# Kernel optimization log

Hardware: AMD Instinct MI355X
Metric: run time of the kernel (lower is better)

## Reference

```python
import jax, jax.numpy as jnp
import numpy as np

B, S, D = 2, 11253, 256
NHEAD, NLEVEL, DFF = 8, 4, 1024
KERNEL = 2
NPOINT = KERNEL * KERNEL
HEAD_DIM = D // NHEAD
LEVEL_SHAPES = [(92, 92), (46, 46), (23, 23), (12, 12)]
LEVEL_STARTS = np.cumsum([0] + [h * w for h, w in LEVEL_SHAPES])[:-1]


def _kernel_indices():
    # BoxeR _create_kernel_indices: even kernel -> [-0.5, 0.5]/K, (x, y) order
    idx = np.arange(KERNEL, dtype=np.float32) - (KERNEL - 1) / 2.0
    i, j = np.meshgrid(idx, idx, indexing="ij")
    return jnp.asarray(np.stack([j, i], -1).reshape(-1, 2) / KERNEL)


KIDX = _kernel_indices()  # (NPOINT, 2) box-relative sample offsets


def layer_norm(x, w, b, eps=1e-5):
    mu = x.mean(-1, keepdims=True)
    var = ((x - mu) ** 2).mean(-1, keepdims=True)
    return (x - mu) * jax.lax.rsqrt(var + eps) * w + b


def setup_inputs() -> dict:
    key = jax.random.key(0)
    ks = jax.random.split(key, 12)

    def p(i, shape, scale=0.02):
        return jax.random.normal(ks[i], shape, jnp.float32) * scale

    cxcy = jax.random.uniform(ks[2], (B, S, 2), jnp.float32, minval=0.1, maxval=0.9)
    wh = jax.random.uniform(ks[3], (B, S, 2), jnp.float32, minval=0.02, maxval=0.2)
    return dict(
        src=jax.random.normal(ks[0], (B, S, D), jnp.float32),
        pos=jax.random.normal(ks[1], (B, S, D), jnp.float32),
        src_shape=jnp.asarray(np.array(LEVEL_SHAPES, np.int32)),
        src_mask=jnp.zeros((B, S), jnp.bool_),
        src_start_index=jnp.asarray(LEVEL_STARTS.astype(np.int32)),
        src_valid_ratios=jnp.ones((B, NLEVEL, 2), jnp.float32),
        ref_windows=jnp.concatenate([cxcy, wh], -1),
        value_w=p(4, (D, D)), value_b=jnp.zeros((D,), jnp.float32),
        out_w=p(5, (D, D)), out_b=jnp.zeros((D,), jnp.float32),
        box_w=p(6, (NHEAD * NLEVEL * 4, D)), box_b=jnp.zeros((NHEAD * NLEVEL * 4,), jnp.float32),
        attn_w=p(7, (NHEAD * NLEVEL * NPOINT, D)), attn_b=jnp.zeros((NHEAD * NLEVEL * NPOINT,), jnp.float32),
        lin1_w=p(8, (DFF, D)), lin1_b=jnp.zeros((DFF,), jnp.float32),
        lin2_w=p(9, (D, DFF)), lin2_b=jnp.zeros((D,), jnp.float32),
        norm1_w=jnp.ones((D,), jnp.float32), norm1_b=jnp.zeros((D,), jnp.float32),
        norm2_w=jnp.ones((D,), jnp.float32), norm2_b=jnp.zeros((D,), jnp.float32),
    )


def box_attention(q, src, src_mask, src_valid_ratios, ref_windows,
                  value_w, value_b, out_w, out_b, box_w, box_b, attn_w, attn_b):
    value = src @ value_w.T + value_b
    value = jnp.where(src_mask[..., None], 0.0, value)
    value = value.reshape(B, S, NHEAD, HEAD_DIM)

    # where-to-attend: per-head, per-level box offsets decoded around ref_windows (cx,cy,w,h)
    off = (q @ box_w.T + box_b).reshape(B, S, NHEAD, NLEVEL, 4)
    ref = ref_windows[:, :, None, None, :]
    boxes = ref + off / 8.0 * ref[..., jnp.array([2, 3, 2, 3])]
    center, size = boxes[..., None, :2], boxes[..., None, 2:]
    grid = center + KIDX * jax.nn.relu(size)  # (B,S,nh,L,P,2) in normalized [0,1] coords
    grid = grid * src_valid_ratios[:, None, None, :, None, :]

    attn = (q @ attn_w.T + attn_b).reshape(B, S, NHEAD, NLEVEL * NPOINT)
    attn = jax.nn.softmax(attn, -1).reshape(B, S, NHEAD, NLEVEL, NPOINT)

    out = jnp.zeros((B, NHEAD, S, HEAD_DIM), src.dtype)
    for lvl, (H, W) in enumerate(LEVEL_SHAPES):
        s0 = int(LEVEL_STARTS[lvl])
        v = jnp.transpose(value[:, s0:s0 + H * W], (0, 2, 1, 3))  # (B,nh,HW,hd)
        loc = jnp.transpose(grid[:, :, :, lvl], (0, 2, 1, 3, 4))  # (B,nh,S,P,2)
        # grid_sample bilinear, align_corners=False, zero padding
        px = loc[..., 0] * W - 0.5
        py = loc[..., 1] * H - 0.5
        x0, y0 = jnp.floor(px), jnp.floor(py)
        wx, wy = (px - x0)[..., None], (py - y0)[..., None]

        def gather(ix, iy):
            valid = (ix >= 0) & (ix < W) & (iy >= 0) & (iy < H)
            idx = (jnp.clip(iy, 0, H - 1) * W + jnp.clip(ix, 0, W - 1)).astype(jnp.int32)
            g = jnp.take_along_axis(v, idx.reshape(B, NHEAD, S * NPOINT)[..., None], axis=2)
            return g.reshape(B, NHEAD, S, NPOINT, HEAD_DIM) * valid[..., None]

        g00, g01 = gather(x0, y0), gather(x0 + 1, y0)
        g10, g11 = gather(x0, y0 + 1), gather(x0 + 1, y0 + 1)
        samp = (g00 * (1 - wx) + g01 * wx) * (1 - wy) + (g10 * (1 - wx) + g11 * wx) * wy
        aw = jnp.transpose(attn[:, :, :, lvl], (0, 2, 1, 3))  # (B,nh,S,P)
        out = out + jnp.einsum("bhspd,bhsp->bhsd", samp, aw)

    out = jnp.transpose(out, (0, 2, 1, 3)).reshape(B, S, D)
    return out @ out_w.T + out_b


def reference(src, pos, src_shape, src_mask, src_start_index, src_valid_ratios,
              ref_windows, value_w, value_b, out_w, out_b, box_w, box_b,
              attn_w, attn_b, lin1_w, lin1_b, lin2_w, lin2_b,
              norm1_w, norm1_b, norm2_w, norm2_b):
    # self-attn (box attention) + residual + LN
    src2 = box_attention(src + pos, src, src_mask, src_valid_ratios, ref_windows,
                         value_w, value_b, out_w, out_b, box_w, box_b, attn_w, attn_b)
    x = layer_norm(src + src2, norm1_w, norm1_b)
    # FFN + residual + LN (dropout=0 in eval)
    ff = jax.nn.relu(x @ lin1_w.T + lin1_b) @ lin2_w.T + lin2_b
    return layer_norm(x + ff, norm2_w, norm2_b)
```

## Files before the change

### kernel.cpp

```cpp
#include <hip/hip_runtime.h>
#include <hip/hip_bf16.h>
#include <hip/hip_fp16.h>

#define TOKENS 22506
#define SLEN   11253

typedef __bf16 bf16x8 __attribute__((ext_vector_type(8)));
typedef float  f32x4  __attribute__((ext_vector_type(4)));
typedef float  f32x2  __attribute__((ext_vector_type(2)));
typedef uint   u32x4  __attribute__((ext_vector_type(4)));
typedef uint   u32x2  __attribute__((ext_vector_type(2)));

#if defined(__has_builtin)
#if __has_builtin(__builtin_amdgcn_cvt_pk_f32_fp8) && __has_builtin(__builtin_amdgcn_cvt_pk_fp8_f32)
#define HAS_FP8CVT 1
#endif
#endif

__device__ __forceinline__ ushort f2bu(float f) {
    __hip_bfloat16 h = __float2bfloat16(f);
    return *reinterpret_cast<ushort*>(&h);
}
__device__ __forceinline__ float bu2f(ushort u) {
    return __uint_as_float((uint)u << 16);
}
__device__ __forceinline__ uint pkf16(float a, float b) {
    __half2 h = __floats2half2_rn(a, b);
    return *reinterpret_cast<uint*>(&h);
}
__device__ __forceinline__ void gl16(const void* g, void* l) {
    __builtin_amdgcn_global_load_lds(
        (__attribute__((address_space(1))) void*)(g),
        (__attribute__((address_space(3))) void*)(l), 16, 0, 0);
}

#ifndef HAS_FP8CVT
__device__ __forceinline__ uint enc_fp8(float x) {
    if (!(fabsf(x) >= 0.f)) return 0;
    uint u = __float_as_uint(x);
    uint s = (u >> 24) & 0x80u;
    float ax = fabsf(x);
    if (ax >= 448.f) return s | 0x7Eu;
    if (ax < 0.0009765625f) return s;
    int e; frexpf(ax, &e);
    int ue = e - 1;
    if (ue < -6) {
        int m = (int)(ax * 512.f + 0.5f);
        if (m > 7) m = 7;
        return s | (uint)m;
    }
    float q = ax * exp2f((float)(3 - ue));
    int mi = (int)(q + 0.5f);
    if (mi >= 16) { mi >>= 1; ++ue; if (ue > 8) return s | 0x7Eu; }
    return s | ((uint)(ue + 7) << 3) | ((uint)mi & 7u);
}
__device__ __forceinline__ float dec_fp8(uint b) {
    const float sgn = (b & 0x80u) ? -1.f : 1.f;
    const uint e = (b >> 3) & 15u, m = b & 7u;
    if (e == 0) return sgn * (float)m * 0.001953125f;
    return sgn * (1.0f + (float)m * 0.125f) * exp2f((float)e - 7.f);
}
#endif

__device__ __forceinline__ uint fp8pack4(float f0, float f1, float f2, float f3) {
#ifdef HAS_FP8CVT
    int p = 0;
    p = __builtin_amdgcn_cvt_pk_fp8_f32(f0, f1, p, false);
    p = __builtin_amdgcn_cvt_pk_fp8_f32(f2, f3, p, true);
    return (uint)p;
#else
    return enc_fp8(f0) | (enc_fp8(f1) << 8) | (enc_fp8(f2) << 16) | (enc_fp8(f3) << 24);
#endif
}
__device__ __forceinline__ uint fp8pack1(float f) {
#ifdef HAS_FP8CVT
    return (uint)__builtin_amdgcn_cvt_pk_fp8_f32(f, f, 0, false) & 0xFFu;
#else
    return enc_fp8(f);
#endif
}
template<bool HI>
__device__ __forceinline__ f32x2 fp8pair(uint w) {
#ifdef HAS_FP8CVT
    auto c = __builtin_amdgcn_cvt_pk_f32_fp8((int)w, HI);
    f32x2 r; r.x = c[0]; r.y = c[1]; return r;
#else
    const uint sh = HI ? 16u : 0u;
    f32x2 r; r.x = dec_fp8((w >> sh) & 0xFFu); r.y = dec_fp8((w >> (sh + 8)) & 0xFFu);
    return r;
#endif
}

__device__ __forceinline__ void xcd_swz(int& bx, int& by) {
    const int nx = gridDim.x, ny = gridDim.y;
    if ((nx & 7) == 0) {
        const int L = blockIdx.x + nx * blockIdx.y;
        const int chunk = nx >> 3;
        const int k = L & 7, j = L >> 3;
        bx = k * chunk + (j % chunk);
        by = j / chunk;
        if (by >= ny) { bx = blockIdx.x; by = blockIdx.y; }
    } else {
        bx = blockIdx.x; by = blockIdx.y;
    }
}

template<bool RELU, bool NTSTORE, bool F8Z0>
__global__ __launch_bounds__(256) void gemm_small(
    const ushort* __restrict__ A0, const ushort* __restrict__ W0,
    const float* __restrict__ b0, void* __restrict__ C0,
    const ushort* __restrict__ A1, const ushort* __restrict__ W1,
    const float* __restrict__ b1, void* __restrict__ C1,
    int M, int N, int K)
{
    const bool zz = blockIdx.z != 0;
    const ushort* A   = zz ? A1 : A0;
    const ushort* W   = zz ? W1 : W0;
    const float* bias = zz ? b1 : b0;
    void* Cptr        = zz ? C1 : C0;

    __shared__ ushort smem[12288];
    const int tid  = threadIdx.x;
    const int lane = tid & 63;
    const int wid  = tid >> 6;
    const int wr = wid >> 1, wc = wid & 1;
    int bx, by; xcd_swz(bx, by);
    const int m0 = bx * 64, n0 = by * 128;
    const int lrow = lane & 15, lhi = lane >> 4;

    const int arow = tid >> 2;
    const int scol = (tid & 3) << 3;
    const ushort* ga  = A + (size_t)min(m0 + arow, M - 1) * K + scol;
    const ushort* gb0 = W + (size_t)(n0 + arow)      * K + scol;
    const ushort* gb1 = W + (size_t)(n0 + arow + 64) * K + scol;

    f32x4 acc[2][4] = {};
    const int NT = K >> 5;

    gl16(ga,  &smem[tid * 8]);
    gl16(gb0, &smem[4096 + tid * 8]);
    gl16(gb1, &smem[4096 + tid * 8 + 2048]);

    int cur = 0;
    for (int t = 0; t < NT; ++t) {
        __syncthreads();
        if (t + 1 < NT) {
            const int k0 = (t + 1) << 5;
            const int nb = cur ^ 1;
            gl16(ga  + k0, &smem[nb * 2048 + tid * 8]);
            gl16(gb0 + k0, &smem[4096 + nb * 4096 + tid * 8]);
            gl16(gb1 + k0, &smem[4096 + nb * 4096 + tid * 8 + 2048]);
        }
        bf16x8 afr[2], bfr[4];
        #pragma unroll
        for (int m = 0; m < 2; ++m)
            afr[m] = *reinterpret_cast<const bf16x8*>(
                &smem[cur * 2048 + (wr * 32 + m * 16 + lrow) * 32 + lhi * 8]);
        #pragma unroll
        for (int n = 0; n < 4; ++n)
            bfr[n] = *reinterpret_cast<const bf16x8*>(
                &smem[4096 + cur * 4096 + (wc * 64 + n * 16 + lrow) * 32 + lhi * 8]);
        #pragma unroll
        for (int m = 0; m < 2; ++m)
            #pragma unroll
            for (int n = 0; n < 4; ++n)
                acc[m][n] = __builtin_amdgcn_mfma_f32_16x16x32_bf16(
                    afr[m], bfr[n], acc[m][n], 0, 0, 0);
        cur ^= 1;
    }

    __syncthreads();
    #pragma unroll
    for (int m = 0; m < 2; ++m) {
        #pragma unroll
        for (int n = 0; n < 4; ++n) {
            const int col = wc * 64 + n * 16 + lrow;
            const float bv = bias[n0 + col];
            #pragma unroll
            for (int r = 0; r < 4; ++r) {
                const int row = wr * 32 + m * 16 + lhi * 4 + r;
                float v = acc[m][n][r] + bv;
                if (RELU) v = fmaxf(v, 0.f);
                smem[row * 136 + col] = f2bu(v);
            }
        }
    }
    __syncthreads();
    if (F8Z0 && !zz) {
        #pragma unroll
        for (int i = 0; i < 4; ++i) {
            const int e = tid + i * 256;
            const int row = e >> 4, ch = e & 15;
            if (m0 + row < M) {
                const u32x4 v = *reinterpret_cast<const u32x4*>(&smem[row * 136 + ch * 8]);
                float f[8];
                #pragma unroll
                for (int j = 0; j < 4; ++j) {
                    f[2 * j]     = __uint_as_float(v[j] << 16);
                    f[2 * j + 1] = __uint_as_float(v[j] & 0xFFFF0000u);
                }
                u32x2 o;
                o[0] = fp8pack4(f[0], f[1], f[2], f[3]);
                o[1] = fp8pack4(f[4], f[5], f[6], f[7]);
                u32x2* dst = reinterpret_cast<u32x2*>(
                    (unsigned char*)Cptr + (size_t)(m0 + row) * N + n0 + ch * 8);
                if (NTSTORE) __builtin_nontemporal_store(o, dst);
                else *dst = o;
            }
        }
    } else {
        #pragma unroll
        for (int i = 0; i < 4; ++i) {
            const int e = tid + i * 256;
            const int row = e >> 4, ch = e & 15;
            if (m0 + row < M) {
                const u32x4 v = *reinterpret_cast<const u32x4*>(&smem[row * 136 + ch * 8]);
                u32x4* dst = reinterpret_cast<u32x4*>(
                    (ushort*)Cptr + (size_t)(m0 + row) * N + n0 + ch * 8);
                if (NTSTORE) __builtin_nontemporal_store(v, dst);
                else *dst = v;
            }
        }
    }
}

__global__ __launch_bounds__(256) void gemm_f8(
    const unsigned char* __restrict__ A, const unsigned char* __restrict__ W,
    const float* __restrict__ bias, ushort* __restrict__ C,
    int M, int N, int K)
{
    __shared__ unsigned char smem[17408];
    const int tid  = threadIdx.x;
    const int lane = tid & 63;
    const int wid  = tid >> 6;
    const int wr = wid >> 1, wc = wid & 1;
    int bx, by; xcd_swz(bx, by);
    const int m0 = bx * 64, n0 = by * 128;
    const int lrow = lane & 15, lhi = lane >> 4;

    const int arow = tid >> 1;
    const int achk = (tid & 1) << 4;
    const unsigned char* ga = A + (size_t)min(m0 + (arow & 63), M - 1) * K + achk;
    const unsigned char* gb = W + (size_t)(n0 + arow) * K + achk;

    f32x4 acc[2][4] = {};
    const int NT = K >> 5;

    if (tid < 128) gl16(ga, &smem[tid * 16]);
    gl16(gb, &smem[4096 + tid * 16]);

    int cur = 0;
    for (int t = 0; t < NT; ++t) {
        __syncthreads();
        if (t + 1 < NT) {
            const int k0 = (t + 1) << 5;
            const int nb = cur ^ 1;
            if (tid < 128) gl16(ga + k0, &smem[nb * 2048 + tid * 16]);
            gl16(gb + k0, &smem[4096 + nb * 4096 + tid * 16]);
        }
        long afr[2], bfr[4];
        #pragma unroll
        for (int m = 0; m < 2; ++m)
            afr[m] = *reinterpret_cast<const long*>(
                &smem[cur * 2048 + (wr * 32 + m * 16 + lrow) * 32 + lhi * 8]);
        #pragma unroll
        for (int n = 0; n < 4; ++n)
            bfr[n] = *reinterpret_cast<const long*>(
                &smem[4096 + cur * 4096 + (wc * 64 + n * 16 + lrow) * 32 + lhi * 8]);
        #pragma unroll
        for (int m = 0; m < 2; ++m)
            #pragma unroll
            for (int n = 0; n < 4; ++n)
                acc[m][n] = __builtin_amdgcn_mfma_f32_16x16x32_fp8_fp8(
                    afr[m], bfr[n], acc[m][n], 0, 0, 0);
        cur ^= 1;
    }

    __syncthreads();
    ushort* sm16 = reinterpret_cast<ushort*>(smem);
    #pragma unroll
    for (int m = 0; m < 2; ++m) {
        #pragma unroll
        for (int n = 0; n < 4; ++n) {
            const int col = wc * 64 + n * 16 + lrow;
            const float bv = bias[n0 + col];
            #pragma unroll
            for (int r = 0; r < 4; ++r) {
                const int row = wr * 32 + m * 16 + lhi * 4 + r;
                sm16[row * 136 + col] = f2bu(acc[m][n][r] + bv);
            }
        }
    }
    __syncthreads();
    #pragma unroll
    for (int i = 0; i < 4; ++i) {
        const int e = tid + i * 256;
        const int row = e >> 4, ch = e & 15;
        if (m0 + row < M) {
            const u32x4 v = *reinterpret_cast<const u32x4*>(&sm16[row * 136 + ch * 8]);
            *reinterpret_cast<u32x4*>(C + (size_t)(m0 + row) * N + n0 + ch * 8) = v;
        }
    }
}

__global__ __launch_bounds__(256) void prep_all(
    const float* __restrict__ vw, const float* __restrict__ bw,
    const float* __restrict__ aw, const float* __restrict__ ow,
    const float* __restrict__ l1, const float* __restrict__ l2,
    const float* __restrict__ bb, const float* __restrict__ ab,
    ushort* __restrict__ dstW, float* __restrict__ dstQB,
    unsigned char* __restrict__ dstW8,
    const float4* __restrict__ src, const float4* __restrict__ pos,
    ushort4* __restrict__ srcb, ushort4* __restrict__ qb)
{
    const int blk = blockIdx.x;
    if (blk < 2817) {
        const int i = blk * 256 + threadIdx.x;
        if (i < 720896) {
            float v;
            if      (i <  65536) v = vw[i];
            else if (i <  98304) v = bw[i -  65536];
            else if (i < 131072) v = aw[i -  98304];
            else if (i < 196608) v = ow[i - 131072];
            else if (i < 458752) v = l1[i - 196608];
            else                 v = l2[i - 458752];
            dstW[i] = f2bu(v);
            if (i >= 458752) dstW8[i - 458752] = (unsigned char)fp8pack1(v);
        } else if (i < 721152) {
            const int j = i - 720896;
            dstQB[j] = (j < 128) ? bb[j] : ab[j - 128];
        }
    } else {
        const int i = (blk - 2817) * 256 + threadIdx.x;
        if (i >= TOKENS * 64) return;
        const float4 s = src[i], p = pos[i];
        ushort4 us, uq;
        us.x = f2bu(s.x); us.y = f2bu(s.y); us.z = f2bu(s.z); us.w = f2bu(s.w);
        uq.x = f2bu(s.x + p.x); uq.y = f2bu(s.y + p.y);
        uq.z = f2bu(s.z + p.z); uq.w = f2bu(s.w + p.w);
        srcb[i] = us; qb[i] = uq;
    }
}

__global__ __launch_bounds__(256) void box_fused(
    const unsigned char* __restrict__ val,
    const ushort* __restrict__ qout,
    const float* __restrict__ refw,
    const float* __restrict__ vratio,
    ushort* __restrict__ attnout)
{
    __shared__ ushort4 offs[64 * 17];
    __shared__ uint2 wts[64 * 17];
    const int tid = threadIdx.x;

    int work;
    {
        const int x = blockIdx.x & 7, s = blockIdx.x >> 3;
        work = (x < 4) ? (s * 4 + x) : (1408 + s * 4 + (x - 4));
        if ((int)gridDim.x != 2814 || work >= (int)gridDim.x) work = blockIdx.x;
    }
    const int t0 = work * 8;

    {
        const int u = tid >> 2, lvl = tid & 3;
        const int t = min(t0 + (u >> 3), TOKENS - 1);
        const int h = u & 7;
        const int b = (t >= SLEN) ? 1 : 0;
        const ushort* qr = qout + (size_t)t * 256;

        const uint2 lu = *reinterpret_cast<const uint2*>(qr + 128 + h * 16 + lvl * 4);
        float e0 = __uint_as_float(lu.x << 16);
        float e1 = __uint_as_float(lu.x & 0xFFFF0000u);
        float e2 = __uint_as_float(lu.y << 16);
        float e3 = __uint_as_float(lu.y & 0xFFFF0000u);
        float mx = fmaxf(fmaxf(e0, e1), fmaxf(e2, e3));
        mx = fmaxf(mx, __shfl_xor(mx, 1));
        mx = fmaxf(mx, __shfl_xor(mx, 2));
        e0 = __expf(e0 - mx); e1 = __expf(e1 - mx);
        e2 = __expf(e2 - mx); e3 = __expf(e3 - mx);
        float ss = e0 + e1 + e2 + e3;
        ss += __shfl_xor(ss, 1);
        ss += __shfl_xor(ss, 2);
        const float inv = 1.f / ss;
        const float pe[4] = { e0 * inv, e1 * inv, e2 * inv, e3 * inv };

        const uint2 ou = *reinterpret_cast<const uint2*>(qr + h * 16 + lvl * 4);
        const float o0 = __uint_as_float(ou.x << 16) * 0.125f;
        const float o1 = __uint_as_float(ou.x & 0xFFFF0000u) * 0.125f;
        const float o2 = __uint_as_float(ou.y << 16) * 0.125f;
        const float o3 = __uint_as_float(ou.y & 0xFFFF0000u) * 0.125f;

        const float4 rw = *reinterpret_cast<const float4*>(refw + (size_t)t * 4);
        const int Ww = (lvl == 0) ? 92 : (lvl == 1) ? 46 : (lvl == 2) ? 23 : 12;
        const int s0 = (lvl == 0) ? 0 : (lvl == 1) ? 8464 : (lvl == 2) ? 10580 : 11109;
        const float vrx = vratio[(b * 4 + lvl) * 2 + 0];
        const float vry = vratio[(b * 4 + lvl) * 2 + 1];

        const float bx  = rw.x + o0 * rw.z;
        const float by  = rw.y + o1 * rw.w;
        const float bwd = fmaxf(rw.z + o2 * rw.z, 0.f);
        const float bhd = fmaxf(rw.w + o3 * rw.w, 0.f);

        #pragma unroll
        for (int k = 0; k < 4; ++k) {
            const float jx = (k & 1) ? 0.25f : -0.25f;
            const float iy = (k & 2) ? 0.25f : -0.25f;
            const float px = (bx + jx * bwd) * vrx * (float)Ww - 0.5f;
            const float py = (by + iy * bhd) * vry * (float)Ww - 0.5f;
            const float x0f = floorf(px), y0f = floorf(py);
            const int x0 = (int)x0f, y0 = (int)y0f;
            const float wx = px - x0f, wy = py - y0f;
            const float wp = pe[k];

            const bool vx0 = (x0 >= 0) && (x0 < Ww);
            const bool vx1 = (x0 + 1 >= 0) && (x0 + 1 < Ww);
            const bool vy0 = (y0 >= 0) && (y0 < Ww);
            const bool vy1 = (y0 + 1 >= 0) && (y0 + 1 < Ww);
            const int cx0 = min(max(x0, 0), Ww - 1);
            const int cx1 = min(max(x0 + 1, 0), Ww - 1);
            const int cy0 = min(max(y0, 0), Ww - 1);
            const int cy1 = min(max(y0 + 1, 0), Ww - 1);

            const float w00 = (vx0 && vy0) ? wp * (1.f - wx) * (1.f - wy) : 0.f;
            const float w01 = (vx1 && vy0) ? wp * wx         * (1.f - wy) : 0.f;
            const float w10 = (vx0 && vy1) ? wp * (1.f - wx) * wy         : 0.f;
            const float w11 = (vx1 && vy1) ? wp * wx         * wy         : 0.f;

            ushort4 sp;
            sp.x = (ushort)(s0 + cy0 * Ww + cx0);
            sp.y = (ushort)(s0 + cy0 * Ww + cx1);
            sp.z = (ushort)(s0 + cy1 * Ww + cx0);
            sp.w = (ushort)(s0 + cy1 * Ww + cx1);

            const int p = lvl * 4 + k;
            offs[u * 17 + p] = sp;
            wts[u * 17 + p]  = make_uint2(pkf16(w00, w01), pkf16(w10, w11));
        }
    }
    __syncthreads();

    const int u = tid >> 2, dl = tid & 3;
    const int hd = dl & 1;
    const int cp = dl >> 1;
    const int traw = t0 + (u >> 3);
    const int t = min(traw, TOKENS - 1);
    const int h = u & 7;
    const uint boff = ((t >= SLEN) ? (uint)SLEN * 256u : 0u)
                    + (uint)h * 32u + (uint)hd * 16u;
    const char* base = (const char*)val;

    const ushort4* po = &offs[u * 17];
    const uint2* pw = &wts[u * 17];
    f32x2 ac0 = {0,0}, ac1 = {0,0}, ac2 = {0,0}, ac3 = {0,0};
    f32x2 ac4 = {0,0}, ac5 = {0,0}, ac6 = {0,0}, ac7 = {0,0};

    #pragma unroll
    for (int g = 0; g < 8; ++g) {
        const ushort4 spA = po[g * 2 + 0];
        const ushort4 spB = po[g * 2 + 1];
        const uint2  wA  = pw[g * 2 + 0];
        const uint2  wB  = pw[g * 2 + 1];

        const uint rA0 = cp ? (uint)spA.z : (uint)spA.x;
        const uint rA1 = cp ? (uint)spA.w : (uint)spA.y;
        const uint rB0 = cp ? (uint)spB.z : (uint)spB.x;
        const uint rB1 = cp ? (uint)spB.w : (uint)spB.y;

        const u32x4 vA0 = *reinterpret_cast<const u32x4*>(base + ((rA0 << 8) + boff));
        const u32x4 vA1 = *reinterpret_cast<const u32x4*>(base + ((rA1 << 8) + boff));
        const u32x4 vB0 = *reinterpret_cast<const u32x4*>(base + ((rB0 << 8) + boff));
        const u32x4 vB1 = *reinterpret_cast<const u32x4*>(base + ((rB1 << 8) + boff));

        const uint wAu = cp ? wA.y : wA.x;
        const uint wBu = cp ? wB.y : wB.x;
        const float2 wAf = __half22float2(*reinterpret_cast<const __half2*>(&wAu));
        const float2 wBf = __half22float2(*reinterpret_cast<const __half2*>(&wBu));

        auto acc16 = [&](const u32x4 v, const float w) {
            f32x2 wv; wv.x = w; wv.y = w;
            ac0 += wv * fp8pair<false>(v[0]);
            ac1 += wv * fp8pair<true >(v[0]);
            ac2 += wv * fp8pair<false>(v[1]);
            ac3 += wv * fp8pair<true >(v[1]);
            ac4 += wv * fp8pair<false>(v[2]);
            ac5 += wv * fp8pair<true >(v[2]);
            ac6 += wv * fp8pair<false>(v[3]);
            ac7 += wv * fp8pair<true >(v[3]);
        };
        acc16(vA0, wAf.x); acc16(vA1, wAf.y);
        acc16(vB0, wBf.x); acc16(vB1, wBf.y);
    }

    auto xsum = [&](f32x2& a) {
        a.x += __shfl_xor(a.x, 2);
        a.y += __shfl_xor(a.y, 2);
    };
    xsum(ac0); xsum(ac1); xsum(ac2); xsum(ac3);
    xsum(ac4); xsum(ac5); xsum(ac6); xsum(ac7);

    if (traw < TOKENS) {
        u32x4 o;
        if (cp == 0) {
            o[0] = (uint)f2bu(ac0.x) | ((uint)f2bu(ac0.y) << 16);
            o[1] = (uint)f2bu(ac1.x) | ((uint)f2bu(ac1.y) << 16);
            o[2] = (uint)f2bu(ac2.x) | ((uint)f2bu(ac2.y) << 16);
            o[3] = (uint)f2bu(ac3.x) | ((uint)f2bu(ac3.y) << 16);
        } else {
            o[0] = (uint)f2bu(ac4.x) | ((uint)f2bu(ac4.y) << 16);
            o[1] = (uint)f2bu(ac5.x) | ((uint)f2bu(ac5.y) << 16);
            o[2] = (uint)f2bu(ac6.x) | ((uint)f2bu(ac6.y) << 16);
            o[3] = (uint)f2bu(ac7.x) | ((uint)f2bu(ac7.y) << 16);
        }
        *reinterpret_cast<u32x4*>(
            attnout + (size_t)t * 256 + h * 32 + hd * 16 + cp * 8) = o;
    }
}

template<bool AF32, bool OUTF32>
__global__ __launch_bounds__(256) void ln_add2(
    const void* __restrict__ aptr, const ushort* __restrict__ bptr,
    const float* __restrict__ w, const float* __restrict__ bias,
    void* __restrict__ outp, int nrows)
{
    const int lane = threadIdx.x & 63, wv = threadIdx.x >> 6;
    const int row = blockIdx.x * 4 + wv;
    if (row >= nrows) return;
    const size_t base = (size_t)row * 256 + lane * 4;

    float4 av;
    if (AF32) {
        av = *reinterpret_cast<const float4*>((const float*)aptr + base);
    } else {
        const ushort4 u = *reinterpret_cast<const ushort4*>((const ushort*)aptr + base);
        av = make_float4(bu2f(u.x), bu2f(u.y), bu2f(u.z), bu2f(u.w));
    }
    const ushort4 ub = *reinterpret_cast<const ushort4*>(bptr + base);
    const float v0 = av.x + bu2f(ub.x), v1 = av.y + bu2f(ub.y);
    const float v2 = av.z + bu2f(ub.z), v3 = av.w + bu2f(ub.w);

    float s = v0 + v1 + v2 + v3;
    #pragma unroll
    for (int o = 32; o; o >>= 1) s += __shfl_xor(s, o);
    const float mu = s * (1.f / 256.f);
    const float d0 = v0 - mu, d1 = v1 - mu, d2 = v2 - mu, d3 = v3 - mu;
    float s2 = d0 * d0 + d1 * d1 + d2 * d2 + d3 * d3;
    #pragma unroll
    for (int o = 32; o; o >>= 1) s2 += __shfl_xor(s2, o);
    const float rs = rsqrtf(s2 * (1.f / 256.f) + 1e-5f);

    const float4 w4 = *reinterpret_cast<const float4*>(w + lane * 4);
    const float4 g4 = *reinterpret_cast<const float4*>(bias + lane * 4);
    const float r0 = d0 * rs * w4.x + g4.x;
    const float r1 = d1 * rs * w4.y + g4.y;
    const float r2 = d2 * rs * w4.z + g4.z;
    const float r3 = d3 * rs * w4.w + g4.w;
    if (OUTF32) {
        *reinterpret_cast<float4*>((float*)outp + base) = make_float4(r0, r1, r2, r3);
    } else {
        ushort4 u;
        u.x = f2bu(r0); u.y = f2bu(r1); u.z = f2bu(r2); u.w = f2bu(r3);
        *reinterpret_cast<ushort4*>((ushort*)outp + base) = u;
    }
}

extern "C" void kernel_launch(void* const* d_in, const int* in_sizes, int n_in,
                              void* d_out, int out_size, void* d_ws, size_t ws_size,
                              hipStream_t stream)
{
    const float* src     = (const float*)d_in[0];
    const float* pos     = (const float*)d_in[1];
    const float* vratio  = (const float*)d_in[5];
    const float* refw    = (const float*)d_in[6];
    const float* value_w = (const float*)d_in[7];
    const float* value_b = (const float*)d_in[8];
    const float* out_w   = (const float*)d_in[9];
    const float* out_b   = (const float*)d_in[10];
    const float* box_w   = (const float*)d_in[11];
    const float* box_b   = (const float*)d_in[12];
    const float* attn_w  = (const float*)d_in[13];
    const float* attn_b  = (const float*)d_in[14];
    const float* lin1_w  = (const float*)d_in[15];
    const float* lin1_b  = (const float*)d_in[16];
    const float* lin2_w  = (const float*)d_in[17];
    const float* lin2_b  = (const float*)d_in[18];
    const float* n1w     = (const float*)d_in[19];
    const float* n1b     = (const float*)d_in[20];
    const float* n2w     = (const float*)d_in[21];
    const float* n2b     = (const float*)d_in[22];

    char* wsb = (char*)d_ws;
    ushort* Wb    = (ushort*)(wsb);
    float*  qcb   = (float*)(wsb + 1441792);
    ushort* srcb  = (ushort*)(wsb + 1442816);
    ushort* qb    = (ushort*)(wsb + 12965888);
    unsigned char* valb = (unsigned char*)(wsb + 24488960);
    ushort* qoutb = (ushort*)(wsb + 36012032);
    ushort* attb  = (ushort*)(wsb + 47535104);
    ushort* src2b = (ushort*)(wsb + 59058176);
    ushort* xbb   = (ushort*)(wsb + 70581248);
    unsigned char* hb8 = (unsigned char*)(wsb + 82104320);
    ushort* yb    = (ushort*)(wsb + 105150464);
    unsigned char* Wf8 = (unsigned char*)(wsb + 116673536);

    const dim3 blk(256);

    prep_all<<<dim3(8444), blk, 0, stream>>>(
        value_w, box_w, attn_w, out_w, lin1_w, lin2_w, box_b, attn_b, Wb, qcb,
        Wf8, (const float4*)src, (const float4*)pos, (ushort4*)srcb, (ushort4*)qb);

    gemm_small<false, false, true><<<dim3(352, 2, 2), blk, 0, stream>>>(
        srcb, Wb, value_b, valb,
        qb, Wb + 65536, qcb, qoutb, TOKENS, 256, 256);

    box_fused<<<dim3((TOKENS + 7) / 8), blk, 0, stream>>>(
        valb, qoutb, refw, vratio, attb);

    gemm_small<false, false, false><<<dim3(352, 2, 1), blk, 0, stream>>>(
        attb, Wb + 131072, out_b, src2b,
        attb, Wb + 131072, out_b, src2b, TOKENS, 256, 256);
    ln_add2<false, false><<<dim3((TOKENS + 3) / 4), blk, 0, stream>>>(
        srcb, src2b, n1w, n1b, xbb, TOKENS);
    gemm_small<true, true, true><<<dim3(352, 8, 1), blk, 0, stream>>>(
        xbb, Wb + 196608, lin1_b, hb8,
        xbb, Wb + 196608, lin1_b, hb8, TOKENS, 1024, 256);
    gemm_f8<<<dim3(352, 2), blk, 0, stream>>>(
        hb8, Wf8, lin2_b, yb, TOKENS, 256, 1024);
    ln_add2<false, true><<<dim3((TOKENS + 3) / 4), blk, 0, stream>>>(
        xbb, yb, n2w, n2b, (float*)d_out, TOKENS);
}
```

Measured before the change: 130.4 us.

## Store FP8 value tensor head-major and gather bilinear row pairs contiguously

The value projection now writes its FP8 output in a (batch, head, token, 32) layout instead of token-major rows. In box attention each lane pair covers one sample column, and the x0/x0+1 neighbours of a head sit 32 bytes apart, so the two corner reads fall in one 64-byte span. Offsets are now stored as two signed 16-bit row starts instead of four clamped indices, and the loads use nontemporal hints. Clamping is dropped, so out-of-range corners rely on their zero weight while still reading addresses that may fall outside the head's block.

```diff
diff --git a/kernel.cpp b/kernel.cpp
--- a/kernel.cpp
+++ b/kernel.cpp
@@ -105,7 +105,7 @@
     }
 }
 
-template<bool RELU, bool NTSTORE, bool F8Z0>
+template<bool RELU, bool NTSTORE, int F8MODE>
 __global__ __launch_bounds__(256) void gemm_small(
     const ushort* __restrict__ A0, const ushort* __restrict__ W0,
     const float* __restrict__ b0, void* __restrict__ C0,
@@ -186,12 +186,13 @@
         }
     }
     __syncthreads();
-    if (F8Z0 && !zz) {
+    if (F8MODE != 0 && (F8MODE == 1 || !zz)) {
         #pragma unroll
         for (int i = 0; i < 4; ++i) {
             const int e = tid + i * 256;
             const int row = e >> 4, ch = e & 15;
-            if (m0 + row < M) {
+            const int grow = m0 + row;
+            if (grow < M) {
                 const u32x4 v = *reinterpret_cast<const u32x4*>(&smem[row * 136 + ch * 8]);
                 float f[8];
                 #pragma unroll
@@ -202,10 +203,20 @@
                 u32x2 o;
                 o[0] = fp8pack4(f[0], f[1], f[2], f[3]);
                 o[1] = fp8pack4(f[4], f[5], f[6], f[7]);
-                u32x2* dst = reinterpret_cast<u32x2*>(
-                    (unsigned char*)Cptr + (size_t)(m0 + row) * N + n0 + ch * 8);
-                if (NTSTORE) __builtin_nontemporal_store(o, dst);
-                else *dst = o;
+                if (F8MODE == 2) {
+                    const int b = grow >= SLEN;
+                    const int s = grow - (b ? SLEN : 0);
+                    const int head = (n0 >> 5) + (ch >> 2);
+                    const int d0 = (ch & 3) * 8;
+                    *reinterpret_cast<u32x2*>(
+                        (unsigned char*)Cptr +
+                        ((size_t)(b * 8 + head) * SLEN + s) * 32 + d0) = o;
+                } else {
+                    u32x2* dst = reinterpret_cast<u32x2*>(
+                        (unsigned char*)Cptr + (size_t)grow * N + n0 + ch * 8);
+                    if (NTSTORE) __builtin_nontemporal_store(o, dst);
+                    else *dst = o;
+                }
             }
         }
     } else {
@@ -349,7 +360,7 @@
     const float* __restrict__ vratio,
     ushort* __restrict__ attnout)
 {
-    __shared__ ushort4 offs[64 * 17];
+    __shared__ uint  offs[64 * 17];
     __shared__ uint2 wts[64 * 17];
     const int tid = threadIdx.x;
 
@@ -416,65 +427,65 @@
             const bool vx1 = (x0 + 1 >= 0) && (x0 + 1 < Ww);
             const bool vy0 = (y0 >= 0) && (y0 < Ww);
             const bool vy1 = (y0 + 1 >= 0) && (y0 + 1 < Ww);
-            const int cx0 = min(max(x0, 0), Ww - 1);
-            const int cx1 = min(max(x0 + 1, 0), Ww - 1);
-            const int cy0 = min(max(y0, 0), Ww - 1);
-            const int cy1 = min(max(y0 + 1, 0), Ww - 1);
 
             const float w00 = (vx0 && vy0) ? wp * (1.f - wx) * (1.f - wy) : 0.f;
             const float w01 = (vx1 && vy0) ? wp * wx         * (1.f - wy) : 0.f;
             const float w10 = (vx0 && vy1) ? wp * (1.f - wx) * wy         : 0.f;
             const float w11 = (vx1 && vy1) ? wp * wx         * wy         : 0.f;
 
-            ushort4 sp;
-            sp.x = (ushort)(s0 + cy0 * Ww + cx0);
-            sp.y = (ushort)(s0 + cy0 * Ww + cx1);
-            sp.z = (ushort)(s0 + cy1 * Ww + cx0);
-            sp.w = (ushort)(s0 + cy1 * Ww + cx1);
+            const int sy0 = s0 + y0 * Ww + x0;
+            const int sy1 = sy0 + Ww;
 
             const int p = lvl * 4 + k;
-            offs[u * 17 + p] = sp;
+            offs[u * 17 + p] = ((uint)(ushort)(short)sy0) |
+                               (((uint)(ushort)(short)sy1) << 16);
             wts[u * 17 + p]  = make_uint2(pkf16(w00, w01), pkf16(w10, w11));
         }
     }
     __syncthreads();
 
     const int u = tid >> 2, dl = tid & 3;
+    const int cx = dl >> 1;
     const int hd = dl & 1;
-    const int cp = dl >> 1;
     const int traw = t0 + (u >> 3);
     const int t = min(traw, TOKENS - 1);
     const int h = u & 7;
-    const uint boff = ((t >= SLEN) ? (uint)SLEN * 256u : 0u)
-                    + (uint)h * 32u + (uint)hd * 16u;
-    const char* base = (const char*)val;
-
-    const ushort4* po = &offs[u * 17];
+    const int b = (t >= SLEN) ? 1 : 0;
+    const char* ubase = (const char*)val +
+        (size_t)(b * 8 + h) * ((size_t)SLEN * 32) + (uint)dl * 16u;
+
+    const uint*  po = &offs[u * 17];
     const uint2* pw = &wts[u * 17];
     f32x2 ac0 = {0,0}, ac1 = {0,0}, ac2 = {0,0}, ac3 = {0,0};
     f32x2 ac4 = {0,0}, ac5 = {0,0}, ac6 = {0,0}, ac7 = {0,0};
 
     #pragma unroll
     for (int g = 0; g < 8; ++g) {
-        const ushort4 spA = po[g * 2 + 0];
-        const ushort4 spB = po[g * 2 + 1];
-        const uint2  wA  = pw[g * 2 + 0];
-        const uint2  wB  = pw[g * 2 + 1];
-
-        const uint rA0 = cp ? (uint)spA.z : (uint)spA.x;
-        const uint rA1 = cp ? (uint)spA.w : (uint)spA.y;
-        const uint rB0 = cp ? (uint)spB.z : (uint)spB.x;
-        const uint rB1 = cp ? (uint)spB.w : (uint)spB.y;
-
-        const u32x4 vA0 = *reinterpret_cast<const u32x4*>(base + ((rA0 << 8) + boff));
-        const u32x4 vA1 = *reinterpret_cast<const u32x4*>(base + ((rA1 << 8) + boff));
-        const u32x4 vB0 = *reinterpret_cast<const u32x4*>(base + ((rB0 << 8) + boff));
-        const u32x4 vB1 = *reinterpret_cast<const u32x4*>(base + ((rB1 << 8) + boff));
-
-        const uint wAu = cp ? wA.y : wA.x;
-        const uint wBu = cp ? wB.y : wB.x;
-        const float2 wAf = __half22float2(*reinterpret_cast<const __half2*>(&wAu));
-        const float2 wBf = __half22float2(*reinterpret_cast<const __half2*>(&wBu));
+        const uint  oA = po[g * 2 + 0];
+        const uint  oB = po[g * 2 + 1];
+        const uint2 wA = pw[g * 2 + 0];
+        const uint2 wB = pw[g * 2 + 1];
+
+        const int sA0 = (short)(oA & 0xFFFFu), sA1 = (short)(oA >> 16);
+        const int sB0 = (short)(oB & 0xFFFFu), sB1 = (short)(oB >> 16);
+
+        const u32x4 vA0 = __builtin_nontemporal_load(
+            reinterpret_cast<const u32x4*>(ubase + (ptrdiff_t)sA0 * 32));
+        const u32x4 vA1 = __builtin_nontemporal_load(
+            reinterpret_cast<const u32x4*>(ubase + (ptrdiff_t)sA1 * 32));
+        const u32x4 vB0 = __builtin_nontemporal_load(
+            reinterpret_cast<const u32x4*>(ubase + (ptrdiff_t)sB0 * 32));
+        const u32x4 vB1 = __builtin_nontemporal_load(
+            reinterpret_cast<const u32x4*>(ubase + (ptrdiff_t)sB1 * 32));
+
+        const float2 wA0 = __half22float2(*reinterpret_cast<const __half2*>(&wA.x));
+        const float2 wA1 = __half22float2(*reinterpret_cast<const __half2*>(&wA.y));
+        const float2 wB0 = __half22float2(*reinterpret_cast<const __half2*>(&wB.x));
+        const float2 wB1 = __half22float2(*reinterpret_cast<const __half2*>(&wB.y));
+        const float fA0 = cx ? wA0.y : wA0.x;
+        const float fA1 = cx ? wA1.y : wA1.x;
+        const float fB0 = cx ? wB0.y : wB0.x;
+        const float fB1 = cx ? wB1.y : wB1.x;
 
         auto acc16 = [&](const u32x4 v, const float w) {
             f32x2 wv; wv.x = w; wv.y = w;
@@ -487,8 +498,8 @@
             ac6 += wv * fp8pair<false>(v[3]);
             ac7 += wv * fp8pair<true >(v[3]);
         };
-        acc16(vA0, wAf.x); acc16(vA1, wAf.y);
-        acc16(vB0, wBf.x); acc16(vB1, wBf.y);
+        acc16(vA0, fA0); acc16(vA1, fA1);
+        acc16(vB0, fB0); acc16(vB1, fB1);
     }
 
     auto xsum = [&](f32x2& a) {
@@ -500,7 +511,7 @@
 
     if (traw < TOKENS) {
         u32x4 o;
-        if (cp == 0) {
+        if (cx == 0) {
             o[0] = (uint)f2bu(ac0.x) | ((uint)f2bu(ac0.y) << 16);
             o[1] = (uint)f2bu(ac1.x) | ((uint)f2bu(ac1.y) << 16);
             o[2] = (uint)f2bu(ac2.x) | ((uint)f2bu(ac2.y) << 16);
@@ -512,7 +523,7 @@
             o[3] = (uint)f2bu(ac7.x) | ((uint)f2bu(ac7.y) << 16);
         }
         *reinterpret_cast<u32x4*>(
-            attnout + (size_t)t * 256 + h * 32 + hd * 16 + cp * 8) = o;
+            attnout + (size_t)t * 256 + h * 32 + hd * 16 + cx * 8) = o;
     }
 }
 
@@ -608,19 +619,19 @@
         value_w, box_w, attn_w, out_w, lin1_w, lin2_w, box_b, attn_b, Wb, qcb,
         Wf8, (const float4*)src, (const float4*)pos, (ushort4*)srcb, (ushort4*)qb);
 
-    gemm_small<false, false, true><<<dim3(352, 2, 2), blk, 0, stream>>>(
+    gemm_small<false, false, 2><<<dim3(352, 2, 2), blk, 0, stream>>>(
         srcb, Wb, value_b, valb,
         qb, Wb + 65536, qcb, qoutb, TOKENS, 256, 256);
 
     box_fused<<<dim3((TOKENS + 7) / 8), blk, 0, stream>>>(
         valb, qoutb, refw, vratio, attb);
 
-    gemm_small<false, false, false><<<dim3(352, 2, 1), blk, 0, stream>>>(
+    gemm_small<false, false, 0><<<dim3(352, 2, 1), blk, 0, stream>>>(
         attb, Wb + 131072, out_b, src2b,
         attb, Wb + 131072, out_b, src2b, TOKENS, 256, 256);
     ln_add2<false, false><<<dim3((TOKENS + 3) / 4), blk, 0, stream>>>(
         srcb, src2b, n1w, n1b, xbb, TOKENS);
-    gemm_small<true, true, true><<<dim3(352, 8, 1), blk, 0, stream>>>(
+    gemm_small<true, true, 1><<<dim3(352, 8, 1), blk, 0, stream>>>(
         xbb, Wb + 196608, lin1_b, hb8,
         xbb, Wb + 196608, lin1_b, hb8, TOKENS, 1024, 256);
     gemm_f8<<<dim3(352, 2), blk, 0, stream>>>(
```

After: 166.6 us. 1.28x slower.
